# Performance work log

Measured on AMD Instinct MI355X. Metric: run time of the kernel, lower is better.

## Reference

```python
import jax, jax.numpy as jnp
import numpy as np

C_FEAT = 32
HIDDEN = 64
R = 4096   # rays (64x64 neural rendering resolution)
S = 96     # depth samples per ray (48 coarse + 48 importance)


def _bilinear_sample(plane, coords):
    # plane: [C,H,W]; coords: [M,2] as (x,y) in [-1,1]
    # torch.F.grid_sample(mode='bilinear', padding_mode='zeros', align_corners=False)
    C, H, W = plane.shape
    x = (coords[:, 0] + 1.0) * (W * 0.5) - 0.5
    y = (coords[:, 1] + 1.0) * (H * 0.5) - 0.5
    x0 = jnp.floor(x)
    y0 = jnp.floor(y)
    wx1 = x - x0
    wy1 = y - y0

    def gather(xi, yi):
        valid = (xi >= 0) & (xi < W) & (yi >= 0) & (yi < H)
        xc = jnp.clip(xi, 0, W - 1).astype(jnp.int32)
        yc = jnp.clip(yi, 0, H - 1).astype(jnp.int32)
        return plane[:, yc, xc] * valid.astype(plane.dtype)[None, :]  # [C,M]

    out = (gather(x0, y0) * (1 - wx1) * (1 - wy1)
           + gather(x0 + 1, y0) * wx1 * (1 - wy1)
           + gather(x0, y0 + 1) * (1 - wx1) * wy1
           + gather(x0 + 1, y0 + 1) * wx1 * wy1)
    return out.T  # [M,C]


def _sample_triplane(planes3, coords):
    # planes3: [3,C,H,W]; coords: [M,3] in [-1,1] (box_warp=2)
    # EG3D plane projections: XY, XZ, ZX
    projs = jnp.stack([coords[:, jnp.array([0, 1])],
                       coords[:, jnp.array([0, 2])],
                       coords[:, jnp.array([2, 0])]], axis=0)  # [3,M,2]
    return jax.vmap(_bilinear_sample)(planes3, projs)  # [3,M,C]


def setup_inputs() -> dict:
    key = jax.random.key(0)
    ks = jax.random.split(key, 7)
    N = 2
    M = R * S
    planes = jax.random.normal(ks[0], (N, 3, C_FEAT, 256, 256), jnp.float32)
    coordinates = jax.random.uniform(ks[1], (N, M, 3), jnp.float32) * 2.0 - 1.0
    depths = jnp.sort(jax.random.uniform(ks[2], (N, R, S, 1), jnp.float32) + 2.0, axis=2)
    w1 = jax.random.normal(ks[3], (HIDDEN, C_FEAT), jnp.float32)
    b1 = jnp.zeros((HIDDEN,), jnp.float32)
    w2 = jax.random.normal(ks[4], (1 + C_FEAT, HIDDEN), jnp.float32)
    b2 = jnp.zeros((1 + C_FEAT,), jnp.float32)
    return {"planes": planes, "coordinates": coordinates, "depths": depths,
            "w1": w1, "b1": b1, "w2": w2, "b2": b2}


def reference(planes, coordinates, depths, w1, b1, w2, b2):
    N = planes.shape[0]
    # --- triplane grid-sample gather: [N,3,M,C] ---
    feats = jax.vmap(_sample_triplane)(planes, coordinates)
    x = feats.mean(axis=1)  # sampled_features.mean(1) -> [N,M,C]

    # --- OSGDecoder (StyleGAN FullyConnectedLayer: runtime weight scale 1/sqrt(fan_in)) ---
    h = jax.nn.softplus(jnp.einsum('nmc,hc->nmh', x, w1) * (1.0 / np.sqrt(C_FEAT)) + b1)
    out = jnp.einsum('nmh,oh->nmo', h, w2) * (1.0 / np.sqrt(HIDDEN)) + b2
    rgb = jax.nn.sigmoid(out[..., 1:]) * (1.0 + 2 * 0.001) - 0.001  # [N,M,32]
    sigma = out[..., 0:1]                                           # [N,M,1]

    # --- NeRF-style ray marcher (MipRayMarcher2, clamp_mode='softplus') ---
    rgb = rgb.reshape(N, R, S, C_FEAT)
    sigma = sigma.reshape(N, R, S, 1)
    deltas = depths[:, :, 1:] - depths[:, :, :-1]            # [N,R,S-1,1]
    colors_mid = 0.5 * (rgb[:, :, :-1] + rgb[:, :, 1:])
    dens_mid = 0.5 * (sigma[:, :, :-1] + sigma[:, :, 1:])
    densities = jax.nn.softplus(dens_mid - 1.0)
    alpha = 1.0 - jnp.exp(-deltas * densities)               # [N,R,S-1,1]
    trans = jnp.cumprod(1.0 - alpha + 1e-10, axis=2)
    trans = jnp.concatenate([jnp.ones_like(trans[:, :, :1]), trans[:, :, :-1]], axis=2)
    weights = alpha * trans
    composite_rgb = jnp.sum(weights * colors_mid, axis=2) * 2.0 - 1.0  # [N,R,32]
    return composite_rgb
```

## Files before the change

kernel.cpp:

```cpp
#include <hip/hip_runtime.h>
#include <hip/hip_fp16.h>

#define NB 2
#define RAYS 4096
#define SAMP 96
#define CF 32
#define HID 64
#define HW 256

constexpr int M_TOTAL = NB * RAYS * SAMP;

typedef _Float16 f16x8 __attribute__((ext_vector_type(8)));
typedef float f32x4 __attribute__((ext_vector_type(4)));
typedef int i32x4 __attribute__((ext_vector_type(4)));

__device__ __forceinline__ float softplus_f(float z) {
    return fmaxf(z, 0.f) + __logf(1.f + __expf(-fabsf(z)));
}
__device__ __forceinline__ float sigmoid_f(float z) {
    return __fdividef(1.f, 1.f + __expf(-z));
}

__global__ __launch_bounds__(256)
void k_transpose(const float* __restrict__ src, __half2* __restrict__ dst) {
    const int i = blockIdx.x * 256 + threadIdx.x;
    const int xy = i & 0xFFFF;
    const int pn = i >> 16;
    const float* s = src + (((size_t)pn * CF) << 16) + xy;
    __half2 v[16];
    #pragma unroll
    for (int c2 = 0; c2 < 16; ++c2) {
        const float a = s[((size_t)(2 * c2)) << 16];
        const float b = s[((size_t)(2 * c2 + 1)) << 16];
        v[c2] = __floats2half2_rn(a, b);
    }
    __half2* d = dst + (size_t)i * 16;
    #pragma unroll
    for (int q = 0; q < 4; ++q)
        ((i32x4*)d)[q] = ((const i32x4*)v)[q];
}

constexpr int TG3 = 192;
constexpr int SLICE_A = 9216;
constexpr int SIGO = 5120;
constexpr int DEPO = 5376;

__global__ __launch_bounds__(TG3)
void k_gmlp3(const __half2* __restrict__ pt, const float* __restrict__ coords,
             const float* __restrict__ depths,
             const float* __restrict__ w1, const float* __restrict__ b1,
             const float* __restrict__ w2, const float* __restrict__ b2,
             float* __restrict__ out)
{
    __shared__ __align__(16) char sm[3 * SLICE_A];
    const int t = threadIdx.x;
    const int wv = t >> 6;
    const int l = t & 63;
    const int g = l >> 4;
    const int ln = l & 15;
    char* const slice = sm + wv * SLICE_A;

    f16x8 b1f[4];
    float b1v[4];
    #pragma unroll
    for (int Nt = 0; Nt < 4; ++Nt) {
        const int hn = 16 * Nt + ln;
        const float4* p0 = (const float4*)(w1 + hn * CF + g * 8);
        float4 u = p0[0], v = p0[1];
        b1f[Nt][0] = (_Float16)u.x; b1f[Nt][1] = (_Float16)u.y;
        b1f[Nt][2] = (_Float16)u.z; b1f[Nt][3] = (_Float16)u.w;
        b1f[Nt][4] = (_Float16)v.x; b1f[Nt][5] = (_Float16)v.y;
        b1f[Nt][6] = (_Float16)v.z; b1f[Nt][7] = (_Float16)v.w;
        b1v[Nt] = b1[hn];
    }
    f16x8 b2f[3][2];
    float b2v[3];
    #pragma unroll
    for (int Nt2 = 0; Nt2 < 3; ++Nt2) {
        const int o = 16 * Nt2 + ln;
        if (o < 33) {
            #pragma unroll
            for (int kh = 0; kh < 2; ++kh) {
                const float4* p0 = (const float4*)(w2 + o * HID + kh * 32 + g * 8);
                float4 u = p0[0], v = p0[1];
                b2f[Nt2][kh][0] = (_Float16)u.x; b2f[Nt2][kh][1] = (_Float16)u.y;
                b2f[Nt2][kh][2] = (_Float16)u.z; b2f[Nt2][kh][3] = (_Float16)u.w;
                b2f[Nt2][kh][4] = (_Float16)v.x; b2f[Nt2][kh][5] = (_Float16)v.y;
                b2f[Nt2][kh][6] = (_Float16)v.z; b2f[Nt2][kh][7] = (_Float16)v.w;
            }
            b2v[Nt2] = b2[o];
        } else {
            #pragma unroll
            for (int kh = 0; kh < 2; ++kh)
                #pragma unroll
                for (int i = 0; i < 8; ++i) b2f[Nt2][kh][i] = (_Float16)0.f;
            b2v[Nt2] = 0.f;
        }
    }

    const int waveBaseS = blockIdx.x * TG3 + wv * 64;
    const int nb = (waveBaseS >= M_TOTAL / NB) ? 1 : 0;
    const __half2* pt_nb = pt + (((size_t)nb * 3) << 16) * 16;
    const __half2 third = __float2half2_rn(1.f / 3.f);
    const float myDep = depths[waveBaseS + l];

    f16x8 a1[4];
    #pragma unroll
    for (int Mt = 0; Mt < 4; ++Mt) {
        const int smp = waveBaseS + 16 * Mt + ln;
        const float* cp = coords + (size_t)smp * 3;
        const float c0 = cp[0], c1 = cp[1], c2v = cp[2];
        __half2 acc4[4];
        #pragma unroll
        for (int j = 0; j < 4; ++j) acc4[j] = __float2half2_rn(0.f);

        #pragma unroll
        for (int p = 0; p < 3; ++p) {
            const float u = (p == 2) ? c2v : c0;
            const float v = (p == 0) ? c1 : ((p == 1) ? c2v : c0);
            const float xf = fmaf(u, 128.f, 127.5f);
            const float yf = fmaf(v, 128.f, 127.5f);
            const float x0f = floorf(xf), y0f = floorf(yf);
            const float wx = xf - x0f, wy = yf - y0f;
            const int x0 = (int)x0f, y0 = (int)y0f;
            const float vx0 = (x0 >= 0 && x0 < HW) ? 1.f : 0.f;
            const float vx1 = (x0 + 1 >= 0 && x0 + 1 < HW) ? 1.f : 0.f;
            const float vy0 = (y0 >= 0 && y0 < HW) ? 1.f : 0.f;
            const float vy1 = (y0 + 1 >= 0 && y0 + 1 < HW) ? 1.f : 0.f;
            const int xc0 = min(max(x0, 0), HW - 1), xc1 = min(max(x0 + 1, 0), HW - 1);
            const int yc0 = min(max(y0, 0), HW - 1), yc1 = min(max(y0 + 1, 0), HW - 1);
            const float w00 = (1.f - wx) * (1.f - wy) * vx0 * vy0;
            const float w10 = wx * (1.f - wy) * vx1 * vy0;
            const float w01 = (1.f - wx) * wy * vx0 * vy1;
            const float w11 = wx * wy * vx1 * vy1;

            const __half2* pb = pt_nb + ((size_t)p << 16) * 16;
            auto tap = [&](int yc, int xc, float w) {
                const float4* tp = (const float4*)(pb + (size_t)(yc * HW + xc) * 16);
                union { float4 f; __half2 h[4]; } u4;
                u4.f = tp[g];
                const __half2 wh = __float2half2_rn(w);
                acc4[0] = __hfma2(wh, u4.h[0], acc4[0]);
                acc4[1] = __hfma2(wh, u4.h[1], acc4[1]);
                acc4[2] = __hfma2(wh, u4.h[2], acc4[2]);
                acc4[3] = __hfma2(wh, u4.h[3], acc4[3]);
            };
            tap(yc0, xc0, w00);
            tap(yc0, xc1, w10);
            tap(yc1, xc0, w01);
            tap(yc1, xc1, w11);
        }
        union { __half2 h[4]; f16x8 f; } uf;
        #pragma unroll
        for (int j = 0; j < 4; ++j) uf.h[j] = __hmul2(acc4[j], third);
        a1[Mt] = uf.f;
    }

    constexpr float is32 = 0.17677669529663687f;
    #pragma unroll
    for (int Nt = 0; Nt < 4; ++Nt) {
        f32x4 d0 = {0.f, 0.f, 0.f, 0.f};
        f32x4 d1 = {0.f, 0.f, 0.f, 0.f};
        f32x4 d2 = {0.f, 0.f, 0.f, 0.f};
        f32x4 d3 = {0.f, 0.f, 0.f, 0.f};
        d0 = __builtin_amdgcn_mfma_f32_16x16x32_f16(a1[0], b1f[Nt], d0, 0, 0, 0);
        d1 = __builtin_amdgcn_mfma_f32_16x16x32_f16(a1[1], b1f[Nt], d1, 0, 0, 0);
        d2 = __builtin_amdgcn_mfma_f32_16x16x32_f16(a1[2], b1f[Nt], d2, 0, 0, 0);
        d3 = __builtin_amdgcn_mfma_f32_16x16x32_f16(a1[3], b1f[Nt], d3, 0, 0, 0);
        const int hcol = 16 * Nt + ln;
        #pragma unroll
        for (int Mt = 0; Mt < 4; ++Mt) {
            f32x4 dd = (Mt == 0) ? d0 : (Mt == 1) ? d1 : (Mt == 2) ? d2 : d3;
            #pragma unroll
            for (int r = 0; r < 4; ++r) {
                const float hv = softplus_f(fmaf(dd[r], is32, b1v[Nt]));
                const int row = 16 * Mt + 4 * g + r;
                *(__half*)(slice + row * 144 + hcol * 2) = __float2half(hv);
            }
        }
    }

    f16x8 a2[4][2];
    #pragma unroll
    for (int Mt = 0; Mt < 4; ++Mt)
        #pragma unroll
        for (int kh = 0; kh < 2; ++kh)
            a2[Mt][kh] = *(const f16x8*)(slice + (16 * Mt + ln) * 144 + (kh * 4 + g) * 16);

    *(float*)(slice + DEPO + l * 4) = myDep;

    #pragma unroll
    for (int Nt2 = 0; Nt2 < 3; ++Nt2) {
        f32x4 e0 = {0.f, 0.f, 0.f, 0.f};
        f32x4 e1 = {0.f, 0.f, 0.f, 0.f};
        f32x4 e2 = {0.f, 0.f, 0.f, 0.f};
        f32x4 e3 = {0.f, 0.f, 0.f, 0.f};
        #pragma unroll
        for (int kh = 0; kh < 2; ++kh) {
            e0 = __builtin_amdgcn_mfma_f32_16x16x32_f16(a2[0][kh], b2f[Nt2][kh], e0, 0, 0, 0);
            e1 = __builtin_amdgcn_mfma_f32_16x16x32_f16(a2[1][kh], b2f[Nt2][kh], e1, 0, 0, 0);
            e2 = __builtin_amdgcn_mfma_f32_16x16x32_f16(a2[2][kh], b2f[Nt2][kh], e2, 0, 0, 0);
            e3 = __builtin_amdgcn_mfma_f32_16x16x32_f16(a2[3][kh], b2f[Nt2][kh], e3, 0, 0, 0);
        }
        const int o = 16 * Nt2 + ln;
        if (o == 0) {
            #pragma unroll
            for (int Mt = 0; Mt < 4; ++Mt) {
                f32x4 ee = (Mt == 0) ? e0 : (Mt == 1) ? e1 : (Mt == 2) ? e2 : e3;
                #pragma unroll
                for (int r = 0; r < 4; ++r) {
                    const int row = 16 * Mt + 4 * g + r;
                    *(float*)(slice + SIGO + row * 4) = fmaf(ee[r], 0.125f, b2v[0]);
                }
            }
        } else if (o < 33) {
            #pragma unroll
            for (int Mt = 0; Mt < 4; ++Mt) {
                f32x4 ee = (Mt == 0) ? e0 : (Mt == 1) ? e1 : (Mt == 2) ? e2 : e3;
                #pragma unroll
                for (int r = 0; r < 4; ++r) {
                    const float vv = fmaf(ee[r], 0.125f, b2v[Nt2]);
                    const float rr = sigmoid_f(vv) * 1.002f - 0.001f;
                    const int row = 16 * Mt + 4 * g + r;
                    *(__half*)(slice + row * 80 + (o - 1) * 2) = __float2half(rr);
                }
            }
        }
    }

    __syncthreads();

    if (t < 64) {
        const int rl = t >> 5;
        const int c = t & 31;
        const int bs = rl * SAMP;
        auto sigAt = [&](int sb) -> float {
            return *(const float*)(sm + (sb >> 6) * SLICE_A + SIGO + (sb & 63) * 4);
        };
        auto depAt = [&](int sb) -> float {
            return *(const float*)(sm + (sb >> 6) * SLICE_A + DEPO + (sb & 63) * 4);
        };
        auto rgbAt = [&](int sb) -> float {
            return __half2float(*(const __half*)(sm + (sb >> 6) * SLICE_A + (sb & 63) * 80 + c * 2));
        };
        float T = 1.f, a_out = 0.f;
        float sp = sigAt(bs), dp = depAt(bs), rp = rgbAt(bs);
        for (int ss = 1; ss < SAMP; ++ss) {
            const float sc = sigAt(bs + ss);
            const float dc = depAt(bs + ss);
            const float rc = rgbAt(bs + ss);
            const float dens = softplus_f(0.5f * (sp + sc) - 1.f);
            const float alpha = 1.f - __expf(-(dc - dp) * dens);
            a_out = fmaf(alpha * T, 0.5f * (rp + rc), a_out);
            T *= 1.f - alpha + 1e-10f;
            sp = sc; dp = dc; rp = rc;
        }
        out[(size_t)(blockIdx.x * 2 + rl) * CF + c] = fmaf(a_out, 2.f, -1.f);
    }
}

constexpr int THREADS = 384;
constexpr int SLICE = 9216;
constexpr int SIG_OFF = 5120;
constexpr int DEP_OFF = 5376;

__global__ __launch_bounds__(THREADS)
void k_fused(const float* __restrict__ planes,
             const float* __restrict__ coords, const float* __restrict__ depths,
             const float* __restrict__ w1, const float* __restrict__ b1,
             const float* __restrict__ w2, const float* __restrict__ b2,
             float* __restrict__ out)
{
    __shared__ __align__(16) char sm[6 * SLICE];
    const int t = threadIdx.x;
    const int wv = t >> 6;
    const int l = t & 63;
    const int g = l >> 4;
    const int ln = l & 15;
    char* const slice = sm + wv * SLICE;

    const int msamp = blockIdx.x * THREADS + t;
    const int nb = (msamp >= M_TOTAL / NB) ? 1 : 0;

    f16x8 b1f[4];
    float b1v[4];
    #pragma unroll
    for (int Nt = 0; Nt < 4; ++Nt) {
        const int hn = 16 * Nt + ln;
        const float4* p0 = (const float4*)(w1 + hn * CF + g * 8);
        float4 u = p0[0], v = p0[1];
        b1f[Nt][0] = (_Float16)u.x; b1f[Nt][1] = (_Float16)u.y;
        b1f[Nt][2] = (_Float16)u.z; b1f[Nt][3] = (_Float16)u.w;
        b1f[Nt][4] = (_Float16)v.x; b1f[Nt][5] = (_Float16)v.y;
        b1f[Nt][6] = (_Float16)v.z; b1f[Nt][7] = (_Float16)v.w;
        b1v[Nt] = b1[hn];
    }
    f16x8 b2f[3][2];
    float b2v[3];
    #pragma unroll
    for (int Nt2 = 0; Nt2 < 3; ++Nt2) {
        const int o = 16 * Nt2 + ln;
        if (o < 33) {
            #pragma unroll
            for (int kh = 0; kh < 2; ++kh) {
                const float4* p0 = (const float4*)(w2 + o * HID + kh * 32 + g * 8);
                float4 u = p0[0], v = p0[1];
                b2f[Nt2][kh][0] = (_Float16)u.x; b2f[Nt2][kh][1] = (_Float16)u.y;
                b2f[Nt2][kh][2] = (_Float16)u.z; b2f[Nt2][kh][3] = (_Float16)u.w;
                b2f[Nt2][kh][4] = (_Float16)v.x; b2f[Nt2][kh][5] = (_Float16)v.y;
                b2f[Nt2][kh][6] = (_Float16)v.z; b2f[Nt2][kh][7] = (_Float16)v.w;
            }
            b2v[Nt2] = b2[o];
        } else {
            #pragma unroll
            for (int kh = 0; kh < 2; ++kh)
                #pragma unroll
                for (int i = 0; i < 8; ++i) b2f[Nt2][kh][i] = (_Float16)0.f;
            b2v[Nt2] = 0.f;
        }
    }

    const float* cp = coords + (size_t)msamp * 3;
    const float c0 = cp[0], c1 = cp[1], c2v = cp[2];
    const float myDep = depths[msamp];

    float xf32[CF];
    #pragma unroll
    for (int c = 0; c < CF; ++c) xf32[c] = 0.f;

    #pragma unroll
    for (int p = 0; p < 3; ++p) {
        const float u = (p == 2) ? c2v : c0;
        const float v = (p == 0) ? c1 : ((p == 1) ? c2v : c0);
        const float xf = fmaf(u, 128.f, 127.5f);
        const float yf = fmaf(v, 128.f, 127.5f);
        const float x0f = floorf(xf), y0f = floorf(yf);
        const float wx = xf - x0f, wy = yf - y0f;
        const int x0 = (int)x0f, y0 = (int)y0f;
        const float vx0 = (x0 >= 0 && x0 < HW) ? 1.f : 0.f;
        const float vx1 = (x0 + 1 >= 0 && x0 + 1 < HW) ? 1.f : 0.f;
        const float vy0 = (y0 >= 0 && y0 < HW) ? 1.f : 0.f;
        const float vy1 = (y0 + 1 >= 0 && y0 + 1 < HW) ? 1.f : 0.f;
        const int xc0 = min(max(x0, 0), HW - 1), xc1 = min(max(x0 + 1, 0), HW - 1);
        const int yc0 = min(max(y0, 0), HW - 1), yc1 = min(max(y0 + 1, 0), HW - 1);
        const float w00 = (1.f - wx) * (1.f - wy) * vx0 * vy0;
        const float w10 = wx * (1.f - wy) * vx1 * vy0;
        const float w01 = (1.f - wx) * wy * vx0 * vy1;
        const float w11 = wx * wy * vx1 * vy1;

        const float* pb = planes + (((size_t)(nb * 3 + p) * CF) << 16);
        const int i00 = yc0 * HW + xc0, i10 = yc0 * HW + xc1;
        const int i01 = yc1 * HW + xc0, i11 = yc1 * HW + xc1;
        #pragma unroll
        for (int c = 0; c < CF; ++c) {
            const float* pc = pb + ((size_t)c << 16);
            float a0 = fmaf(w00, pc[i00], fmaf(w10, pc[i10], 0.f));
            float a1 = fmaf(w01, pc[i01], fmaf(w11, pc[i11], 0.f));
            xf32[c] += a0 + a1;
        }
    }

    #pragma unroll
    for (int c = 0; c < 4; ++c) {
        union { __half2 h[4]; i32x4 v; } u4;
        #pragma unroll
        for (int j = 0; j < 4; ++j)
            u4.h[j] = __floats2half2_rn(xf32[8 * c + 2 * j] * (1.f / 3.f),
                                        xf32[8 * c + 2 * j + 1] * (1.f / 3.f));
        *(i32x4*)(slice + l * 80 + c * 16) = u4.v;
    }

    f16x8 a1[4];
    #pragma unroll
    for (int Mt = 0; Mt < 4; ++Mt)
        a1[Mt] = *(const f16x8*)(slice + (16 * Mt + ln) * 80 + g * 16);

    constexpr float is32 = 0.17677669529663687f;
    #pragma unroll
    for (int Nt = 0; Nt < 4; ++Nt) {
        f32x4 d0 = {0.f, 0.f, 0.f, 0.f};
        f32x4 d1 = {0.f, 0.f, 0.f, 0.f};
        f32x4 d2 = {0.f, 0.f, 0.f, 0.f};
        f32x4 d3 = {0.f, 0.f, 0.f, 0.f};
        d0 = __builtin_amdgcn_mfma_f32_16x16x32_f16(a1[0], b1f[Nt], d0, 0, 0, 0);
        d1 = __builtin_amdgcn_mfma_f32_16x16x32_f16(a1[1], b1f[Nt], d1, 0, 0, 0);
        d2 = __builtin_amdgcn_mfma_f32_16x16x32_f16(a1[2], b1f[Nt], d2, 0, 0, 0);
        d3 = __builtin_amdgcn_mfma_f32_16x16x32_f16(a1[3], b1f[Nt], d3, 0, 0, 0);
        const int hcol = 16 * Nt + ln;
        #pragma unroll
        for (int Mt = 0; Mt < 4; ++Mt) {
            f32x4 dd = (Mt == 0) ? d0 : (Mt == 1) ? d1 : (Mt == 2) ? d2 : d3;
            #pragma unroll
            for (int r = 0; r < 4; ++r) {
                const float hv = softplus_f(fmaf(dd[r], is32, b1v[Nt]));
                const int row = 16 * Mt + 4 * g + r;
                *(__half*)(slice + row * 144 + hcol * 2) = __float2half(hv);
            }
        }
    }

    f16x8 a2[4][2];
    #pragma unroll
    for (int Mt = 0; Mt < 4; ++Mt)
        #pragma unroll
        for (int kh = 0; kh < 2; ++kh)
            a2[Mt][kh] = *(const f16x8*)(slice + (16 * Mt + ln) * 144 + (kh * 4 + g) * 16);

    *(float*)(slice + DEP_OFF + l * 4) = myDep;

    #pragma unroll
    for (int Nt2 = 0; Nt2 < 3; ++Nt2) {
        f32x4 e0 = {0.f, 0.f, 0.f, 0.f};
        f32x4 e1 = {0.f, 0.f, 0.f, 0.f};
        f32x4 e2 = {0.f, 0.f, 0.f, 0.f};
        f32x4 e3 = {0.f, 0.f, 0.f, 0.f};
        #pragma unroll
        for (int kh = 0; kh < 2; ++kh) {
            e0 = __builtin_amdgcn_mfma_f32_16x16x32_f16(a2[0][kh], b2f[Nt2][kh], e0, 0, 0, 0);
            e1 = __builtin_amdgcn_mfma_f32_16x16x32_f16(a2[1][kh], b2f[Nt2][kh], e1, 0, 0, 0);
            e2 = __builtin_amdgcn_mfma_f32_16x16x32_f16(a2[2][kh], b2f[Nt2][kh], e2, 0, 0, 0);
            e3 = __builtin_amdgcn_mfma_f32_16x16x32_f16(a2[3][kh], b2f[Nt2][kh], e3, 0, 0, 0);
        }
        const int o = 16 * Nt2 + ln;
        if (o == 0) {
            #pragma unroll
            for (int Mt = 0; Mt < 4; ++Mt) {
                f32x4 ee = (Mt == 0) ? e0 : (Mt == 1) ? e1 : (Mt == 2) ? e2 : e3;
                #pragma unroll
                for (int r = 0; r < 4; ++r) {
                    const int row = 16 * Mt + 4 * g + r;
                    *(float*)(slice + SIG_OFF + row * 4) = fmaf(ee[r], 0.125f, b2v[0]);
                }
            }
        } else if (o < 33) {
            #pragma unroll
            for (int Mt = 0; Mt < 4; ++Mt) {
                f32x4 ee = (Mt == 0) ? e0 : (Mt == 1) ? e1 : (Mt == 2) ? e2 : e3;
                #pragma unroll
                for (int r = 0; r < 4; ++r) {
                    const float vv = fmaf(ee[r], 0.125f, b2v[Nt2]);
                    const float rr = sigmoid_f(vv) * 1.002f - 0.001f;
                    const int row = 16 * Mt + 4 * g + r;
                    *(__half*)(slice + row * 80 + (o + 1) * 2) = __float2half(rr);
                }
            }
        }
    }

    __syncthreads();

    if (t < 128) {
        const int crl = t >> 5;
        const int c = t & 31;
        const int bs = crl * SAMP;
        auto sigAt = [&](int sb) -> float {
            return *(const float*)(sm + (sb >> 6) * SLICE + SIG_OFF + (sb & 63) * 4);
        };
        auto depAt = [&](int sb) -> float {
            return *(const float*)(sm + (sb >> 6) * SLICE + DEP_OFF + (sb & 63) * 4);
        };
        auto rgbAt = [&](int sb) -> float {
            return __half2float(*(const __half*)(sm + (sb >> 6) * SLICE + (sb & 63) * 80 + (c + 1) * 2));
        };
        float T = 1.f, a_out = 0.f;
        float sp = sigAt(bs), dp = depAt(bs), rp = rgbAt(bs);
        for (int ss = 1; ss < SAMP; ++ss) {
            const float sc = sigAt(bs + ss);
            const float dc = depAt(bs + ss);
            const float rc = rgbAt(bs + ss);
            const float dens = softplus_f(0.5f * (sp + sc) - 1.f);
            const float alpha = 1.f - __expf(-(dc - dp) * dens);
            a_out = fmaf(alpha * T, 0.5f * (rp + rc), a_out);
            T *= 1.f - alpha + 1e-10f;
            sp = sc; dp = dc; rp = rc;
        }
        out[(size_t)(blockIdx.x * 4 + crl) * CF + c] = fmaf(a_out, 2.f, -1.f);
    }
}

extern "C" void kernel_launch(void* const* d_in, const int* in_sizes, int n_in,
                              void* d_out, int out_size, void* d_ws, size_t ws_size,
                              hipStream_t stream) {
    (void)in_sizes; (void)n_in; (void)out_size;
    const float* planes = (const float*)d_in[0];
    const float* coords = (const float*)d_in[1];
    const float* depths = (const float*)d_in[2];
    const float* w1 = (const float*)d_in[3];
    const float* b1 = (const float*)d_in[4];
    const float* w2 = (const float*)d_in[5];
    const float* b2 = (const float*)d_in[6];
    float* out = (float*)d_out;

    const size_t ptBytes = (size_t)NB * 3 * HW * HW * CF * sizeof(__half);
    const int tgrid = NB * 3 * HW * HW / 256;

    if (ws_size >= ptBytes) {
        __half2* pt = (__half2*)d_ws;
        k_transpose<<<tgrid, 256, 0, stream>>>(planes, pt);
        k_gmlp3<<<M_TOTAL / TG3, TG3, 0, stream>>>(pt, coords, depths,
                                                   w1, b1, w2, b2, out);
    } else {
        k_fused<<<M_TOTAL / THREADS, THREADS, 0, stream>>>(planes, coords, depths,
                                                           w1, b1, w2, b2, out);
    }
}
```

Measured before the change: 171.8 us.

## Pad triplane layout to drop bounds checks and split compositing into separate kernel

The transposed triplane gets a one-texel zero border (258x258), so the bilinear gather needs no validity masks or clamps and the taps become fixed offsets from one base pointer. The 1/3 plane average is folded into the first-layer weight scale. When workspace allows, the fused kernel is split into a 128-thread gather+MLP kernel that writes fp16 rgb and fp32 sigma to workspace, plus a separate ray-compositing kernel that prefetches the next sample. This removes the 192-thread block constraint and the idle waves during compositing, at the cost of extra global traffic for the intermediate buffers and an additional kernel launch.

```diff
diff --git a/kernel.cpp b/kernel.cpp
--- a/kernel.cpp
+++ b/kernel.cpp
@@ -7,6 +7,8 @@
 #define CF 32
 #define HID 64
 #define HW 256
+#define PW 258
+#define PTEX (PW * PW)
 
 constexpr int M_TOTAL = NB * RAYS * SAMP;
 
@@ -22,35 +24,291 @@
 }
 
 __global__ __launch_bounds__(256)
-void k_transpose(const float* __restrict__ src, __half2* __restrict__ dst) {
-    const int i = blockIdx.x * 256 + threadIdx.x;
-    const int xy = i & 0xFFFF;
-    const int pn = i >> 16;
-    const float* s = src + (((size_t)pn * CF) << 16) + xy;
+void k_transposeB(const float* __restrict__ src, __half2* __restrict__ dst) {
+    const int xy = blockIdx.x * 256 + threadIdx.x;
+    const int pn = blockIdx.y;
+    if (xy >= PTEX) return;
+    const int y = xy / PW;
+    const int x = xy - y * PW;
     __half2 v[16];
-    #pragma unroll
-    for (int c2 = 0; c2 < 16; ++c2) {
-        const float a = s[((size_t)(2 * c2)) << 16];
-        const float b = s[((size_t)(2 * c2 + 1)) << 16];
-        v[c2] = __floats2half2_rn(a, b);
-    }
-    __half2* d = dst + (size_t)i * 16;
+    if (x >= 1 && x <= HW && y >= 1 && y <= HW) {
+        const float* s = src + (((size_t)pn * CF) << 16) + (y - 1) * HW + (x - 1);
+        #pragma unroll
+        for (int c2 = 0; c2 < 16; ++c2) {
+            const float a = s[((size_t)(2 * c2)) << 16];
+            const float b = s[((size_t)(2 * c2 + 1)) << 16];
+            v[c2] = __floats2half2_rn(a, b);
+        }
+    } else {
+        #pragma unroll
+        for (int c2 = 0; c2 < 16; ++c2) v[c2] = __float2half2_rn(0.f);
+    }
+    __half2* d = dst + ((size_t)pn * PTEX + xy) * 16;
     #pragma unroll
     for (int q = 0; q < 4; ++q)
         ((i32x4*)d)[q] = ((const i32x4*)v)[q];
 }
 
-constexpr int TG3 = 192;
+struct Wreg {
+    f16x8 b1f[4];  float b1v[4];
+    f16x8 b2f[3][2]; float b2v[3];
+};
+
+__device__ __forceinline__ void load_weights(Wreg& w,
+        const float* __restrict__ w1, const float* __restrict__ b1,
+        const float* __restrict__ w2, const float* __restrict__ b2,
+        int g, int ln) {
+    #pragma unroll
+    for (int Nt = 0; Nt < 4; ++Nt) {
+        const int hn = 16 * Nt + ln;
+        const float4* p0 = (const float4*)(w1 + hn * CF + g * 8);
+        float4 u = p0[0], v = p0[1];
+        w.b1f[Nt][0] = (_Float16)u.x; w.b1f[Nt][1] = (_Float16)u.y;
+        w.b1f[Nt][2] = (_Float16)u.z; w.b1f[Nt][3] = (_Float16)u.w;
+        w.b1f[Nt][4] = (_Float16)v.x; w.b1f[Nt][5] = (_Float16)v.y;
+        w.b1f[Nt][6] = (_Float16)v.z; w.b1f[Nt][7] = (_Float16)v.w;
+        w.b1v[Nt] = b1[hn];
+    }
+    #pragma unroll
+    for (int Nt2 = 0; Nt2 < 3; ++Nt2) {
+        const int o = 16 * Nt2 + ln;
+        if (o < 33) {
+            #pragma unroll
+            for (int kh = 0; kh < 2; ++kh) {
+                const float4* p0 = (const float4*)(w2 + o * HID + kh * 32 + g * 8);
+                float4 u = p0[0], v = p0[1];
+                w.b2f[Nt2][kh][0] = (_Float16)u.x; w.b2f[Nt2][kh][1] = (_Float16)u.y;
+                w.b2f[Nt2][kh][2] = (_Float16)u.z; w.b2f[Nt2][kh][3] = (_Float16)u.w;
+                w.b2f[Nt2][kh][4] = (_Float16)v.x; w.b2f[Nt2][kh][5] = (_Float16)v.y;
+                w.b2f[Nt2][kh][6] = (_Float16)v.z; w.b2f[Nt2][kh][7] = (_Float16)v.w;
+            }
+            w.b2v[Nt2] = b2[o];
+        } else {
+            #pragma unroll
+            for (int kh = 0; kh < 2; ++kh)
+                #pragma unroll
+                for (int i = 0; i < 8; ++i) w.b2f[Nt2][kh][i] = (_Float16)0.f;
+            w.b2v[Nt2] = 0.f;
+        }
+    }
+}
+
+__device__ __forceinline__ f16x8 gather4(const __half* __restrict__ ptb,
+                                         const float* __restrict__ cp, int g) {
+    const float c0 = cp[0], c1 = cp[1], c2v = cp[2];
+    __half2 acc4[4];
+    #pragma unroll
+    for (int j = 0; j < 4; ++j) acc4[j] = __float2half2_rn(0.f);
+
+    #pragma unroll
+    for (int p = 0; p < 3; ++p) {
+        const float u = (p == 2) ? c2v : c0;
+        const float v = (p == 0) ? c1 : ((p == 1) ? c2v : c0);
+        const float xf = fmaf(u, 128.f, 127.5f);
+        const float yf = fmaf(v, 128.f, 127.5f);
+        const float x0f = floorf(xf), y0f = floorf(yf);
+        const float wx = xf - x0f, wy = yf - y0f;
+        const int x0 = (int)x0f, y0 = (int)y0f;
+        const int base = (y0 + 1) * PW + (x0 + 1);
+        const __half* tp = ptb + (size_t)p * (PTEX * CF) + (size_t)base * CF + g * 8;
+        const float w00 = (1.f - wx) * (1.f - wy);
+        const float w10 = wx * (1.f - wy);
+        const float w01 = (1.f - wx) * wy;
+        const float w11 = wx * wy;
+        auto tapf = [&](const __half* q, float w) {
+            union { float4 f; __half2 h[4]; } u4;
+            u4.f = *(const float4*)q;
+            const __half2 wh = __float2half2_rn(w);
+            acc4[0] = __hfma2(wh, u4.h[0], acc4[0]);
+            acc4[1] = __hfma2(wh, u4.h[1], acc4[1]);
+            acc4[2] = __hfma2(wh, u4.h[2], acc4[2]);
+            acc4[3] = __hfma2(wh, u4.h[3], acc4[3]);
+        };
+        tapf(tp, w00);
+        tapf(tp + CF, w10);
+        tapf(tp + PW * CF, w01);
+        tapf(tp + PW * CF + CF, w11);
+    }
+    union { __half2 h[4]; f16x8 f; } uf;
+    #pragma unroll
+    for (int j = 0; j < 4; ++j) uf.h[j] = acc4[j];
+    return uf.f;
+}
+
 constexpr int SLICE_A = 9216;
 constexpr int SIGO = 5120;
 constexpr int DEPO = 5376;
-
-__global__ __launch_bounds__(TG3)
-void k_gmlp3(const __half2* __restrict__ pt, const float* __restrict__ coords,
-             const float* __restrict__ depths,
+constexpr float IS32_3 = 0.058925565098879624f;
+
+__device__ __forceinline__ void mlp_slice(char* slice, const f16x8 a1[4],
+                                          const Wreg& w, int g, int ln) {
+    #pragma unroll
+    for (int Nt = 0; Nt < 4; ++Nt) {
+        f32x4 d0 = {0.f, 0.f, 0.f, 0.f};
+        f32x4 d1 = {0.f, 0.f, 0.f, 0.f};
+        f32x4 d2 = {0.f, 0.f, 0.f, 0.f};
+        f32x4 d3 = {0.f, 0.f, 0.f, 0.f};
+        d0 = __builtin_amdgcn_mfma_f32_16x16x32_f16(a1[0], w.b1f[Nt], d0, 0, 0, 0);
+        d1 = __builtin_amdgcn_mfma_f32_16x16x32_f16(a1[1], w.b1f[Nt], d1, 0, 0, 0);
+        d2 = __builtin_amdgcn_mfma_f32_16x16x32_f16(a1[2], w.b1f[Nt], d2, 0, 0, 0);
+        d3 = __builtin_amdgcn_mfma_f32_16x16x32_f16(a1[3], w.b1f[Nt], d3, 0, 0, 0);
+        const int hcol = 16 * Nt + ln;
+        #pragma unroll
+        for (int Mt = 0; Mt < 4; ++Mt) {
+            f32x4 dd = (Mt == 0) ? d0 : (Mt == 1) ? d1 : (Mt == 2) ? d2 : d3;
+            #pragma unroll
+            for (int r = 0; r < 4; ++r) {
+                const float hv = softplus_f(fmaf(dd[r], IS32_3, w.b1v[Nt]));
+                const int row = 16 * Mt + 4 * g + r;
+                *(__half*)(slice + row * 144 + hcol * 2) = __float2half(hv);
+            }
+        }
+    }
+
+    f16x8 a2[4][2];
+    #pragma unroll
+    for (int Mt = 0; Mt < 4; ++Mt)
+        #pragma unroll
+        for (int kh = 0; kh < 2; ++kh)
+            a2[Mt][kh] = *(const f16x8*)(slice + (16 * Mt + ln) * 144 + (kh * 4 + g) * 16);
+
+    #pragma unroll
+    for (int Nt2 = 0; Nt2 < 3; ++Nt2) {
+        f32x4 e0 = {0.f, 0.f, 0.f, 0.f};
+        f32x4 e1 = {0.f, 0.f, 0.f, 0.f};
+        f32x4 e2 = {0.f, 0.f, 0.f, 0.f};
+        f32x4 e3 = {0.f, 0.f, 0.f, 0.f};
+        #pragma unroll
+        for (int kh = 0; kh < 2; ++kh) {
+            e0 = __builtin_amdgcn_mfma_f32_16x16x32_f16(a2[0][kh], w.b2f[Nt2][kh], e0, 0, 0, 0);
+            e1 = __builtin_amdgcn_mfma_f32_16x16x32_f16(a2[1][kh], w.b2f[Nt2][kh], e1, 0, 0, 0);
+            e2 = __builtin_amdgcn_mfma_f32_16x16x32_f16(a2[2][kh], w.b2f[Nt2][kh], e2, 0, 0, 0);
+            e3 = __builtin_amdgcn_mfma_f32_16x16x32_f16(a2[3][kh], w.b2f[Nt2][kh], e3, 0, 0, 0);
+        }
+        const int o = 16 * Nt2 + ln;
+        if (o == 0) {
+            #pragma unroll
+            for (int Mt = 0; Mt < 4; ++Mt) {
+                f32x4 ee = (Mt == 0) ? e0 : (Mt == 1) ? e1 : (Mt == 2) ? e2 : e3;
+                #pragma unroll
+                for (int r = 0; r < 4; ++r) {
+                    const int row = 16 * Mt + 4 * g + r;
+                    *(float*)(slice + SIGO + row * 4) = fmaf(ee[r], 0.125f, w.b2v[0]);
+                }
+            }
+        } else if (o < 33) {
+            #pragma unroll
+            for (int Mt = 0; Mt < 4; ++Mt) {
+                f32x4 ee = (Mt == 0) ? e0 : (Mt == 1) ? e1 : (Mt == 2) ? e2 : e3;
+                #pragma unroll
+                for (int r = 0; r < 4; ++r) {
+                    const float vv = fmaf(ee[r], 0.125f, w.b2v[Nt2]);
+                    const float rr = sigmoid_f(vv) * 1.002f - 0.001f;
+                    const int row = 16 * Mt + 4 * g + r;
+                    *(__half*)(slice + row * 80 + (o - 1) * 2) = __float2half(rr);
+                }
+            }
+        }
+    }
+}
+
+constexpr int TG = 128;
+
+__global__ __launch_bounds__(TG)
+void k_gmlpB(const __half2* __restrict__ pt, const float* __restrict__ coords,
              const float* __restrict__ w1, const float* __restrict__ b1,
              const float* __restrict__ w2, const float* __restrict__ b2,
-             float* __restrict__ out)
+             __half* __restrict__ rgbW, float* __restrict__ sigW)
+{
+    __shared__ __align__(16) char sm[(TG / 64) * SLICE_A];
+    const int t = threadIdx.x;
+    const int wv = t >> 6;
+    const int l = t & 63;
+    const int g = l >> 4;
+    const int ln = l & 15;
+    char* const slice = sm + wv * SLICE_A;
+
+    Wreg w;
+    load_weights(w, w1, b1, w2, b2, g, ln);
+
+    const int waveBaseS = blockIdx.x * TG + wv * 64;
+    const int nb = (waveBaseS >= M_TOTAL / NB) ? 1 : 0;
+    const __half* ptb = (const __half*)pt + (size_t)nb * 3 * (PTEX * CF);
+
+    f16x8 a1[4];
+    #pragma unroll
+    for (int Mt = 0; Mt < 4; ++Mt) {
+        const int smp = waveBaseS + 16 * Mt + ln;
+        a1[Mt] = gather4(ptb, coords + (size_t)smp * 3, g);
+    }
+
+    mlp_slice(slice, a1, w, g, ln);
+
+    const int q0 = l & 3, r0 = l >> 2;
+    #pragma unroll
+    for (int q = 0; q < 4; ++q) {
+        const int row = 16 * q + r0;
+        i32x4 v = *(const i32x4*)(slice + row * 80 + q0 * 16);
+        __builtin_nontemporal_store(v,
+            (i32x4*)((char*)rgbW + (size_t)(waveBaseS + row) * 64 + q0 * 16));
+    }
+    const float sv = *(const float*)(slice + SIGO + l * 4);
+    __builtin_nontemporal_store(sv, sigW + waveBaseS + l);
+}
+
+__global__ __launch_bounds__(512)
+void k_comp(const __half* __restrict__ rgbW, const float* __restrict__ sigW,
+            const float* __restrict__ depths, float* __restrict__ out)
+{
+    __shared__ float sgS[16 * SAMP];
+    __shared__ float dpS[16 * SAMP];
+    const int t = threadIdx.x;
+    const int rayBase = blockIdx.x * 16;
+    for (int i = t; i < 16 * SAMP; i += 512) {
+        sgS[i] = sigW[(size_t)rayBase * SAMP + i];
+        dpS[i] = depths[(size_t)rayBase * SAMP + i];
+    }
+    __syncthreads();
+
+    const int rs = t >> 5;
+    const int c = t & 31;
+    const size_t mb = (size_t)(rayBase + rs) * SAMP;
+    const ushort* rgbU = (const ushort*)rgbW;
+
+    auto ldr = [&](size_t idx) -> float {
+        ushort u = __builtin_nontemporal_load(rgbU + idx);
+        __half h = *(__half*)&u;
+        return __half2float(h);
+    };
+
+    float T = 1.f, a_out = 0.f;
+    float sp = sgS[rs * SAMP], dp = dpS[rs * SAMP];
+    float rp = ldr(mb * 32 + c);
+    float rnx = ldr((mb + 1) * 32 + c);
+    #pragma unroll 2
+    for (int ss = 1; ss < SAMP; ++ss) {
+        const float rc = rnx;
+        const int nxt = (ss + 1 < SAMP) ? (ss + 1) : (SAMP - 1);
+        rnx = ldr((mb + nxt) * 32 + c);
+        const float sc = sgS[rs * SAMP + ss];
+        const float dc = dpS[rs * SAMP + ss];
+        const float dens = softplus_f(0.5f * (sp + sc) - 1.f);
+        const float alpha = 1.f - __expf(-(dc - dp) * dens);
+        a_out = fmaf(alpha * T, 0.5f * (rp + rc), a_out);
+        T *= 1.f - alpha + 1e-10f;
+        sp = sc; dp = dc; rp = rc;
+    }
+    out[(size_t)(rayBase + rs) * CF + c] = fmaf(a_out, 2.f, -1.f);
+}
+
+constexpr int TG3 = 192;
+
+__global__ __launch_bounds__(TG3)
+void k_gmlp3B(const __half2* __restrict__ pt, const float* __restrict__ coords,
+              const float* __restrict__ depths,
+              const float* __restrict__ w1, const float* __restrict__ b1,
+              const float* __restrict__ w2, const float* __restrict__ b2,
+              float* __restrict__ out)
 {
     __shared__ __align__(16) char sm[3 * SLICE_A];
     const int t = threadIdx.x;
@@ -60,173 +318,23 @@
     const int ln = l & 15;
     char* const slice = sm + wv * SLICE_A;
 
-    f16x8 b1f[4];
-    float b1v[4];
-    #pragma unroll
-    for (int Nt = 0; Nt < 4; ++Nt) {
-        const int hn = 16 * Nt + ln;
-        const float4* p0 = (const float4*)(w1 + hn * CF + g * 8);
-        float4 u = p0[0], v = p0[1];
-        b1f[Nt][0] = (_Float16)u.x; b1f[Nt][1] = (_Float16)u.y;
-        b1f[Nt][2] = (_Float16)u.z; b1f[Nt][3] = (_Float16)u.w;
-        b1f[Nt][4] = (_Float16)v.x; b1f[Nt][5] = (_Float16)v.y;
-        b1f[Nt][6] = (_Float16)v.z; b1f[Nt][7] = (_Float16)v.w;
-        b1v[Nt] = b1[hn];
-    }
-    f16x8 b2f[3][2];
-    float b2v[3];
-    #pragma unroll
-    for (int Nt2 = 0; Nt2 < 3; ++Nt2) {
-        const int o = 16 * Nt2 + ln;
-        if (o < 33) {
-            #pragma unroll
-            for (int kh = 0; kh < 2; ++kh) {
-                const float4* p0 = (const float4*)(w2 + o * HID + kh * 32 + g * 8);
-                float4 u = p0[0], v = p0[1];
-                b2f[Nt2][kh][0] = (_Float16)u.x; b2f[Nt2][kh][1] = (_Float16)u.y;
-                b2f[Nt2][kh][2] = (_Float16)u.z; b2f[Nt2][kh][3] = (_Float16)u.w;
-                b2f[Nt2][kh][4] = (_Float16)v.x; b2f[Nt2][kh][5] = (_Float16)v.y;
-                b2f[Nt2][kh][6] = (_Float16)v.z; b2f[Nt2][kh][7] = (_Float16)v.w;
-            }
-            b2v[Nt2] = b2[o];
-        } else {
-            #pragma unroll
-            for (int kh = 0; kh < 2; ++kh)
-                #pragma unroll
-                for (int i = 0; i < 8; ++i) b2f[Nt2][kh][i] = (_Float16)0.f;
-            b2v[Nt2] = 0.f;
-        }
-    }
+    Wreg w;
+    load_weights(w, w1, b1, w2, b2, g, ln);
 
     const int waveBaseS = blockIdx.x * TG3 + wv * 64;
     const int nb = (waveBaseS >= M_TOTAL / NB) ? 1 : 0;
-    const __half2* pt_nb = pt + (((size_t)nb * 3) << 16) * 16;
-    const __half2 third = __float2half2_rn(1.f / 3.f);
+    const __half* ptb = (const __half*)pt + (size_t)nb * 3 * (PTEX * CF);
     const float myDep = depths[waveBaseS + l];
 
     f16x8 a1[4];
     #pragma unroll
     for (int Mt = 0; Mt < 4; ++Mt) {
         const int smp = waveBaseS + 16 * Mt + ln;
-        const float* cp = coords + (size_t)smp * 3;
-        const float c0 = cp[0], c1 = cp[1], c2v = cp[2];
-        __half2 acc4[4];
-        #pragma unroll
-        for (int j = 0; j < 4; ++j) acc4[j] = __float2half2_rn(0.f);
-
-        #pragma unroll
-        for (int p = 0; p < 3; ++p) {
-            const float u = (p == 2) ? c2v : c0;
-            const float v = (p == 0) ? c1 : ((p == 1) ? c2v : c0);
-            const float xf = fmaf(u, 128.f, 127.5f);
-            const float yf = fmaf(v, 128.f, 127.5f);
-            const float x0f = floorf(xf), y0f = floorf(yf);
-            const float wx = xf - x0f, wy = yf - y0f;
-            const int x0 = (int)x0f, y0 = (int)y0f;
-            const float vx0 = (x0 >= 0 && x0 < HW) ? 1.f : 0.f;
-            const float vx1 = (x0 + 1 >= 0 && x0 + 1 < HW) ? 1.f : 0.f;
-            const float vy0 = (y0 >= 0 && y0 < HW) ? 1.f : 0.f;
-            const float vy1 = (y0 + 1 >= 0 && y0 + 1 < HW) ? 1.f : 0.f;
-            const int xc0 = min(max(x0, 0), HW - 1), xc1 = min(max(x0 + 1, 0), HW - 1);
-            const int yc0 = min(max(y0, 0), HW - 1), yc1 = min(max(y0 + 1, 0), HW - 1);
-            const float w00 = (1.f - wx) * (1.f - wy) * vx0 * vy0;
-            const float w10 = wx * (1.f - wy) * vx1 * vy0;
-            const float w01 = (1.f - wx) * wy * vx0 * vy1;
-            const float w11 = wx * wy * vx1 * vy1;
-
-            const __half2* pb = pt_nb + ((size_t)p << 16) * 16;
-            auto tap = [&](int yc, int xc, float w) {
-                const float4* tp = (const float4*)(pb + (size_t)(yc * HW + xc) * 16);
-                union { float4 f; __half2 h[4]; } u4;
-                u4.f = tp[g];
-                const __half2 wh = __float2half2_rn(w);
-                acc4[0] = __hfma2(wh, u4.h[0], acc4[0]);
-                acc4[1] = __hfma2(wh, u4.h[1], acc4[1]);
-                acc4[2] = __hfma2(wh, u4.h[2], acc4[2]);
-                acc4[3] = __hfma2(wh, u4.h[3], acc4[3]);
-            };
-            tap(yc0, xc0, w00);
-            tap(yc0, xc1, w10);
-            tap(yc1, xc0, w01);
-            tap(yc1, xc1, w11);
-        }
-        union { __half2 h[4]; f16x8 f; } uf;
-        #pragma unroll
-        for (int j = 0; j < 4; ++j) uf.h[j] = __hmul2(acc4[j], third);
-        a1[Mt] = uf.f;
-    }
-
-    constexpr float is32 = 0.17677669529663687f;
-    #pragma unroll
-    for (int Nt = 0; Nt < 4; ++Nt) {
-        f32x4 d0 = {0.f, 0.f, 0.f, 0.f};
-        f32x4 d1 = {0.f, 0.f, 0.f, 0.f};
-        f32x4 d2 = {0.f, 0.f, 0.f, 0.f};
-        f32x4 d3 = {0.f, 0.f, 0.f, 0.f};
-        d0 = __builtin_amdgcn_mfma_f32_16x16x32_f16(a1[0], b1f[Nt], d0, 0, 0, 0);
-        d1 = __builtin_amdgcn_mfma_f32_16x16x32_f16(a1[1], b1f[Nt], d1, 0, 0, 0);
-        d2 = __builtin_amdgcn_mfma_f32_16x16x32_f16(a1[2], b1f[Nt], d2, 0, 0, 0);
-        d3 = __builtin_amdgcn_mfma_f32_16x16x32_f16(a1[3], b1f[Nt], d3, 0, 0, 0);
-        const int hcol = 16 * Nt + ln;
-        #pragma unroll
-        for (int Mt = 0; Mt < 4; ++Mt) {
-            f32x4 dd = (Mt == 0) ? d0 : (Mt == 1) ? d1 : (Mt == 2) ? d2 : d3;
-            #pragma unroll
-            for (int r = 0; r < 4; ++r) {
-                const float hv = softplus_f(fmaf(dd[r], is32, b1v[Nt]));
-                const int row = 16 * Mt + 4 * g + r;
-                *(__half*)(slice + row * 144 + hcol * 2) = __float2half(hv);
-            }
-        }
-    }
-
-    f16x8 a2[4][2];
-    #pragma unroll
-    for (int Mt = 0; Mt < 4; ++Mt)
-        #pragma unroll
-        for (int kh = 0; kh < 2; ++kh)
-            a2[Mt][kh] = *(const f16x8*)(slice + (16 * Mt + ln) * 144 + (kh * 4 + g) * 16);
-
+        a1[Mt] = gather4(ptb, coords + (size_t)smp * 3, g);
+    }
+
+    mlp_slice(slice, a1, w, g, ln);
     *(float*)(slice + DEPO + l * 4) = myDep;
-
-    #pragma unroll
-    for (int Nt2 = 0; Nt2 < 3; ++Nt2) {
-        f32x4 e0 = {0.f, 0.f, 0.f, 0.f};
-        f32x4 e1 = {0.f, 0.f, 0.f, 0.f};
-        f32x4 e2 = {0.f, 0.f, 0.f, 0.f};
-        f32x4 e3 = {0.f, 0.f, 0.f, 0.f};
-        #pragma unroll
-        for (int kh = 0; kh < 2; ++kh) {
-            e0 = __builtin_amdgcn_mfma_f32_16x16x32_f16(a2[0][kh], b2f[Nt2][kh], e0, 0, 0, 0);
-            e1 = __builtin_amdgcn_mfma_f32_16x16x32_f16(a2[1][kh], b2f[Nt2][kh], e1, 0, 0, 0);
-            e2 = __builtin_amdgcn_mfma_f32_16x16x32_f16(a2[2][kh], b2f[Nt2][kh], e2, 0, 0, 0);
-            e3 = __builtin_amdgcn_mfma_f32_16x16x32_f16(a2[3][kh], b2f[Nt2][kh], e3, 0, 0, 0);
-        }
-        const int o = 16 * Nt2 + ln;
-        if (o == 0) {
-            #pragma unroll
-            for (int Mt = 0; Mt < 4; ++Mt) {
-                f32x4 ee = (Mt == 0) ? e0 : (Mt == 1) ? e1 : (Mt == 2) ? e2 : e3;
-                #pragma unroll
-                for (int r = 0; r < 4; ++r) {
-                    const int row = 16 * Mt + 4 * g + r;
-                    *(float*)(slice + SIGO + row * 4) = fmaf(ee[r], 0.125f, b2v[0]);
-                }
-            }
-        } else if (o < 33) {
-            #pragma unroll
-            for (int Mt = 0; Mt < 4; ++Mt) {
-                f32x4 ee = (Mt == 0) ? e0 : (Mt == 1) ? e1 : (Mt == 2) ? e2 : e3;
-                #pragma unroll
-                for (int r = 0; r < 4; ++r) {
-                    const float vv = fmaf(ee[r], 0.125f, b2v[Nt2]);
-                    const float rr = sigmoid_f(vv) * 1.002f - 0.001f;
-                    const int row = 16 * Mt + 4 * g + r;
-                    *(__half*)(slice + row * 80 + (o - 1) * 2) = __float2half(rr);
-                }
-            }
-        }
-    }
 
     __syncthreads();
 
@@ -282,43 +390,8 @@
     const int msamp = blockIdx.x * THREADS + t;
     const int nb = (msamp >= M_TOTAL / NB) ? 1 : 0;
 
-    f16x8 b1f[4];
-    float b1v[4];
-    #pragma unroll
-    for (int Nt = 0; Nt < 4; ++Nt) {
-        const int hn = 16 * Nt + ln;
-        const float4* p0 = (const float4*)(w1 + hn * CF + g * 8);
-        float4 u = p0[0], v = p0[1];
-        b1f[Nt][0] = (_Float16)u.x; b1f[Nt][1] = (_Float16)u.y;
-        b1f[Nt][2] = (_Float16)u.z; b1f[Nt][3] = (_Float16)u.w;
-        b1f[Nt][4] = (_Float16)v.x; b1f[Nt][5] = (_Float16)v.y;
-        b1f[Nt][6] = (_Float16)v.z; b1f[Nt][7] = (_Float16)v.w;
-        b1v[Nt] = b1[hn];
-    }
-    f16x8 b2f[3][2];
-    float b2v[3];
-    #pragma unroll
-    for (int Nt2 = 0; Nt2 < 3; ++Nt2) {
-        const int o = 16 * Nt2 + ln;
-        if (o < 33) {
-            #pragma unroll
-            for (int kh = 0; kh < 2; ++kh) {
-                const float4* p0 = (const float4*)(w2 + o * HID + kh * 32 + g * 8);
-                float4 u = p0[0], v = p0[1];
-                b2f[Nt2][kh][0] = (_Float16)u.x; b2f[Nt2][kh][1] = (_Float16)u.y;
-                b2f[Nt2][kh][2] = (_Float16)u.z; b2f[Nt2][kh][3] = (_Float16)u.w;
-                b2f[Nt2][kh][4] = (_Float16)v.x; b2f[Nt2][kh][5] = (_Float16)v.y;
-                b2f[Nt2][kh][6] = (_Float16)v.z; b2f[Nt2][kh][7] = (_Float16)v.w;
-            }
-            b2v[Nt2] = b2[o];
-        } else {
-            #pragma unroll
-            for (int kh = 0; kh < 2; ++kh)
-                #pragma unroll
-                for (int i = 0; i < 8; ++i) b2f[Nt2][kh][i] = (_Float16)0.f;
-            b2v[Nt2] = 0.f;
-        }
-    }
+    Wreg w;
+    load_weights(w, w1, b1, w2, b2, g, ln);
 
     const float* cp = coords + (size_t)msamp * 3;
     const float c0 = cp[0], c1 = cp[1], c2v = cp[2];
@@ -355,8 +428,8 @@
         for (int c = 0; c < CF; ++c) {
             const float* pc = pb + ((size_t)c << 16);
             float a0 = fmaf(w00, pc[i00], fmaf(w10, pc[i10], 0.f));
-            float a1 = fmaf(w01, pc[i01], fmaf(w11, pc[i11], 0.f));
-            xf32[c] += a0 + a1;
+            float a1v = fmaf(w01, pc[i01], fmaf(w11, pc[i11], 0.f));
+            xf32[c] += a0 + a1v;
         }
     }
 
@@ -365,8 +438,7 @@
         union { __half2 h[4]; i32x4 v; } u4;
         #pragma unroll
         for (int j = 0; j < 4; ++j)
-            u4.h[j] = __floats2half2_rn(xf32[8 * c + 2 * j] * (1.f / 3.f),
-                                        xf32[8 * c + 2 * j + 1] * (1.f / 3.f));
+            u4.h[j] = __floats2half2_rn(xf32[8 * c + 2 * j], xf32[8 * c + 2 * j + 1]);
         *(i32x4*)(slice + l * 80 + c * 16) = u4.v;
     }
 
@@ -375,77 +447,8 @@
     for (int Mt = 0; Mt < 4; ++Mt)
         a1[Mt] = *(const f16x8*)(slice + (16 * Mt + ln) * 80 + g * 16);
 
-    constexpr float is32 = 0.17677669529663687f;
-    #pragma unroll
-    for (int Nt = 0; Nt < 4; ++Nt) {
-        f32x4 d0 = {0.f, 0.f, 0.f, 0.f};
-        f32x4 d1 = {0.f, 0.f, 0.f, 0.f};
-        f32x4 d2 = {0.f, 0.f, 0.f, 0.f};
-        f32x4 d3 = {0.f, 0.f, 0.f, 0.f};
-        d0 = __builtin_amdgcn_mfma_f32_16x16x32_f16(a1[0], b1f[Nt], d0, 0, 0, 0);
-        d1 = __builtin_amdgcn_mfma_f32_16x16x32_f16(a1[1], b1f[Nt], d1, 0, 0, 0);
-        d2 = __builtin_amdgcn_mfma_f32_16x16x32_f16(a1[2], b1f[Nt], d2, 0, 0, 0);
-        d3 = __builtin_amdgcn_mfma_f32_16x16x32_f16(a1[3], b1f[Nt], d3, 0, 0, 0);
-        const int hcol = 16 * Nt + ln;
-        #pragma unroll
-        for (int Mt = 0; Mt < 4; ++Mt) {
-            f32x4 dd = (Mt == 0) ? d0 : (Mt == 1) ? d1 : (Mt == 2) ? d2 : d3;
-            #pragma unroll
-            for (int r = 0; r < 4; ++r) {
-                const float hv = softplus_f(fmaf(dd[r], is32, b1v[Nt]));
-                const int row = 16 * Mt + 4 * g + r;
-                *(__half*)(slice + row * 144 + hcol * 2) = __float2half(hv);
-            }
-        }
-    }
-
-    f16x8 a2[4][2];
-    #pragma unroll
-    for (int Mt = 0; Mt < 4; ++Mt)
-        #pragma unroll
-        for (int kh = 0; kh < 2; ++kh)
-            a2[Mt][kh] = *(const f16x8*)(slice + (16 * Mt + ln) * 144 + (kh * 4 + g) * 16);
-
+    mlp_slice(slice, a1, w, g, ln);
     *(float*)(slice + DEP_OFF + l * 4) = myDep;
-
-    #pragma unroll
-    for (int Nt2 = 0; Nt2 < 3; ++Nt2) {
-        f32x4 e0 = {0.f, 0.f, 0.f, 0.f};
-        f32x4 e1 = {0.f, 0.f, 0.f, 0.f};
-        f32x4 e2 = {0.f, 0.f, 0.f, 0.f};
-        f32x4 e3 = {0.f, 0.f, 0.f, 0.f};
-        #pragma unroll
-        for (int kh = 0; kh < 2; ++kh) {
-            e0 = __builtin_amdgcn_mfma_f32_16x16x32_f16(a2[0][kh], b2f[Nt2][kh], e0, 0, 0, 0);
-            e1 = __builtin_amdgcn_mfma_f32_16x16x32_f16(a2[1][kh], b2f[Nt2][kh], e1, 0, 0, 0);
-            e2 = __builtin_amdgcn_mfma_f32_16x16x32_f16(a2[2][kh], b2f[Nt2][kh], e2, 0, 0, 0);
-            e3 = __builtin_amdgcn_mfma_f32_16x16x32_f16(a2[3][kh], b2f[Nt2][kh], e3, 0, 0, 0);
-        }
-        const int o = 16 * Nt2 + ln;
-        if (o == 0) {
-            #pragma unroll
-            for (int Mt = 0; Mt < 4; ++Mt) {
-                f32x4 ee = (Mt == 0) ? e0 : (Mt == 1) ? e1 : (Mt == 2) ? e2 : e3;
-                #pragma unroll
-                for (int r = 0; r < 4; ++r) {
-                    const int row = 16 * Mt + 4 * g + r;
-                    *(float*)(slice + SIG_OFF + row * 4) = fmaf(ee[r], 0.125f, b2v[0]);
-                }
-            }
-        } else if (o < 33) {
-            #pragma unroll
-            for (int Mt = 0; Mt < 4; ++Mt) {
-                f32x4 ee = (Mt == 0) ? e0 : (Mt == 1) ? e1 : (Mt == 2) ? e2 : e3;
-                #pragma unroll
-                for (int r = 0; r < 4; ++r) {
-                    const float vv = fmaf(ee[r], 0.125f, b2v[Nt2]);
-                    const float rr = sigmoid_f(vv) * 1.002f - 0.001f;
-                    const int row = 16 * Mt + 4 * g + r;
-                    *(__half*)(slice + row * 80 + (o + 1) * 2) = __float2half(rr);
-                }
-            }
-        }
-    }
 
     __syncthreads();
 
@@ -460,7 +463,7 @@
             return *(const float*)(sm + (sb >> 6) * SLICE + DEP_OFF + (sb & 63) * 4);
         };
         auto rgbAt = [&](int sb) -> float {
-            return __half2float(*(const __half*)(sm + (sb >> 6) * SLICE + (sb & 63) * 80 + (c + 1) * 2));
+            return __half2float(*(const __half*)(sm + (sb >> 6) * SLICE + (sb & 63) * 80 + c * 2));
         };
         float T = 1.f, a_out = 0.f;
         float sp = sigAt(bs), dp = depAt(bs), rp = rgbAt(bs);
@@ -491,14 +494,24 @@
     const float* b2 = (const float*)d_in[6];
     float* out = (float*)d_out;
 
-    const size_t ptBytes = (size_t)NB * 3 * HW * HW * CF * sizeof(__half);
-    const int tgrid = NB * 3 * HW * HW / 256;
-
-    if (ws_size >= ptBytes) {
+    const size_t ptBytes  = (size_t)NB * 3 * PTEX * CF * sizeof(__half);
+    const size_t rgbBytes = (size_t)M_TOTAL * CF * sizeof(__half);
+    const size_t sigBytes = (size_t)M_TOTAL * sizeof(float);
+
+    dim3 tgrid((PTEX + 255) / 256, NB * 3);
+
+    if (ws_size >= ptBytes + rgbBytes + sigBytes) {
         __half2* pt = (__half2*)d_ws;
-        k_transpose<<<tgrid, 256, 0, stream>>>(planes, pt);
-        k_gmlp3<<<M_TOTAL / TG3, TG3, 0, stream>>>(pt, coords, depths,
-                                                   w1, b1, w2, b2, out);
+        __half* rgbW = (__half*)((char*)d_ws + ptBytes);
+        float* sigW = (float*)((char*)d_ws + ptBytes + rgbBytes);
+        k_transposeB<<<tgrid, 256, 0, stream>>>(planes, pt);
+        k_gmlpB<<<M_TOTAL / TG, TG, 0, stream>>>(pt, coords, w1, b1, w2, b2, rgbW, sigW);
+        k_comp<<<NB * RAYS / 16, 512, 0, stream>>>(rgbW, sigW, depths, out);
+    } else if (ws_size >= ptBytes) {
+        __half2* pt = (__half2*)d_ws;
+        k_transposeB<<<tgrid, 256, 0, stream>>>(planes, pt);
+        k_gmlp3B<<<M_TOTAL / TG3, TG3, 0, stream>>>(pt, coords, depths,
+                                                    w1, b1, w2, b2, out);
     } else {
         k_fused<<<M_TOTAL / THREADS, THREADS, 0, stream>>>(planes, coords, depths,
                                                            w1, b1, w2, b2, out);
```

Result: slower. 179.3 us (+4.3%).
